# Performance work log

Hardware: AMD Instinct MI355X
Metric: run time of the kernel (lower is better)

Reference implementation:

```python
import jax, jax.numpy as jnp
import numpy as np

D_MODEL = 1024
NUM_HEADS = 16
D_STATE = D_MODEL // NUM_HEADS
BS, SEQ = 8, 1024
NEG_BIG = 1e10


def setup_inputs() -> dict:
    key = jax.random.key(0)
    ks = jax.random.split(key, 3)
    std = 0.02
    x = jax.random.normal(ks[0], (BS, SEQ, D_MODEL), dtype=jnp.float32)
    qkv_w = jax.random.normal(ks[1], (D_MODEL, 3 * D_MODEL), dtype=jnp.float32) * std
    qkv_b = jnp.zeros((3 * D_MODEL,), dtype=jnp.float32)
    out_w = jax.random.normal(ks[2], (D_MODEL, D_MODEL), dtype=jnp.float32) * std
    out_b = jnp.zeros((D_MODEL,), dtype=jnp.float32)
    return {"x": x, "qkv_w": qkv_w, "qkv_b": qkv_b, "out_w": out_w, "out_b": out_b}


def reference(x, qkv_w, qkv_b, out_w, out_b):
    bs, n, d = x.shape
    qkv = jnp.matmul(x, qkv_w) + qkv_b  # [bs, n, 3*d_model]
    q, k, v = jnp.split(qkv, 3, axis=-1)

    def split_heads(t):  # [bs, n, d] -> [bs, h, n, d_state]
        return t.reshape(bs, n, NUM_HEADS, D_STATE).transpose(0, 2, 1, 3)

    q, k, v = split_heads(q), split_heads(k), split_heads(v)
    scale = 1.0 / np.sqrt(D_STATE).astype(np.float32)
    scores = jnp.einsum('bhqd,bhkd->bhqk', q, k) * scale  # [bs,h,n,n]
    # causal mask: i >= j (mask(n) with ns==nd)
    m = (jnp.arange(n)[:, None] >= jnp.arange(n)[None, :]).astype(scores.dtype)
    scores = scores * m - (1.0 - m) * NEG_BIG
    attn = jax.nn.softmax(scores, axis=-1)
    out = jnp.einsum('bhqk,bhkd->bhqd', attn, v)  # [bs,h,n,d_state]
    out = out.transpose(0, 2, 1, 3).reshape(bs, n, d)
    return jnp.matmul(out, out_w) + out_b
```

## Files before the change

### kernel.cpp

```cpp
#include <hip/hip_runtime.h>
#include <hip/hip_bf16.h>
#include <stdint.h>

typedef __attribute__((ext_vector_type(8))) __bf16 bf16x8;
typedef __attribute__((ext_vector_type(4))) float f32x4;
typedef __attribute__((ext_vector_type(4))) unsigned int u32x4;
typedef __attribute__((ext_vector_type(4))) unsigned short u16x4;

#define SEQ 1024
#define DM 1024

#if __has_builtin(__builtin_amdgcn_exp2f)
#define EXP2(x) __builtin_amdgcn_exp2f(x)
#else
#define EXP2(x) exp2f(x)
#endif

typedef __attribute__((address_space(3))) void lds_t;
typedef __attribute__((address_space(1))) void glb_t;

__device__ __forceinline__ unsigned short f2bf(float f){
  __hip_bfloat16 h = __float2bfloat16(f);
  return __builtin_bit_cast(unsigned short, h);
}
__device__ __forceinline__ bf16x8 ld16(const unsigned short* p){
  u32x4 v = *(const u32x4*)p;
  return __builtin_bit_cast(bf16x8, v);
}
__device__ __forceinline__ void gload_lds16(const unsigned short* g, unsigned short* l){
  __builtin_amdgcn_global_load_lds((const glb_t*)g, (lds_t*)l, 16, 0, 0);
}

__global__ void cvt_f32_bf16(const float* __restrict__ in,
                             unsigned short* __restrict__ out, int n)
{
  int i = (blockIdx.x * blockDim.x + threadIdx.x) * 8;
  if (i >= n) return;
  float4 a = *(const float4*)(in + i);
  float4 b = *(const float4*)(in + i + 4);
  unsigned short v[8] = { f2bf(a.x), f2bf(a.y), f2bf(a.z), f2bf(a.w),
                          f2bf(b.x), f2bf(b.y), f2bf(b.z), f2bf(b.w) };
  *(u32x4*)(out + i) = *(u32x4*)v;
}

__global__ void transpose_cvt(const float* __restrict__ in,
                              unsigned short* __restrict__ out, int R, int C)
{
  __shared__ unsigned short t[32][33];
  int x  = blockIdx.x * 32 + threadIdx.x;
  int y0 = blockIdx.y * 32 + threadIdx.y;
#pragma unroll
  for (int i = 0; i < 32; i += 8)
    t[threadIdx.y + i][threadIdx.x] = f2bf(in[(size_t)(y0 + i) * C + x]);
  __syncthreads();
  int ox  = blockIdx.y * 32 + threadIdx.x;
  int oy0 = blockIdx.x * 32 + threadIdx.y;
#pragma unroll
  for (int i = 0; i < 32; i += 8)
    out[(size_t)(oy0 + i) * R + ox] = t[threadIdx.x][threadIdx.y + i];
}

template <int MODE>
__global__ __launch_bounds__(256, 3)
void gemm_bt(const unsigned short* __restrict__ A,
             const unsigned short* __restrict__ Bt,
             const float* __restrict__ bias,
             void* __restrict__ C0, unsigned short* __restrict__ vT,
             int M, int N, int K)
{
  __shared__ unsigned short Ls[3][2][128 * 32];
  const int tid = threadIdx.x;
  const int l = tid & 63;
  const int w = tid >> 6;

  const int nbn = N >> 7;
  const int nwg = gridDim.x;
  const int bid = blockIdx.x;
  const int qq  = nwg >> 3;
  const int sb  = (bid & 7) * qq + (bid >> 3);
  const int bm = sb / nbn, bn = sb % nbn;
  const int row0 = bm << 7, col0 = bn << 7;

  const int rA = w * 16 + (l >> 2);
  const int cS = ((l & 3) ^ ((l >> 3) & 3)) * 8;
  const unsigned short* ag = A  + (size_t)(row0 + rA) * K + cS;
  const unsigned short* bg = Bt + (size_t)(col0 + rA) * K + cS;

  auto STAGE = [&](int kt, int bi) {
    const unsigned short* a = ag + kt * 32;
    const unsigned short* b = bg + kt * 32;
    gload_lds16(a,                  &Ls[bi][0][w * 512]);
    gload_lds16(a + (size_t)64 * K, &Ls[bi][0][2048 + w * 512]);
    gload_lds16(b,                  &Ls[bi][1][w * 512]);
    gload_lds16(b + (size_t)64 * K, &Ls[bi][1][2048 + w * 512]);
  };

  const int wr = (w >> 1) * 64, wc = (w & 1) * 64;
  const f32x4 zz = {0.f, 0.f, 0.f, 0.f};
  f32x4 acc[4][4];
#pragma unroll
  for (int m = 0; m < 4; m++)
#pragma unroll
    for (int n = 0; n < 4; n++) acc[m][n] = zz;

  const int c16 = l & 15;
  const int csw = ((l >> 4) * 8) ^ (((l >> 1) & 3) << 3);

  const int NT = K >> 5;
  STAGE(0, 0);
  STAGE(1, 1);
  asm volatile("s_waitcnt vmcnt(4)" ::: "memory");
  __builtin_amdgcn_s_barrier();

  int cur = 0, stg = 2;
  for (int kt = 0; kt < NT; kt++) {
    if (kt + 2 < NT) STAGE(kt + 2, stg);

    const unsigned short* La = &Ls[cur][0][0];
    const unsigned short* Lb = &Ls[cur][1][0];
    bf16x8 af[4], bfr[4];
#pragma unroll
    for (int m = 0; m < 4; m++)
      af[m] = ld16(La + (wr + m * 16 + c16) * 32 + csw);
#pragma unroll
    for (int n = 0; n < 4; n++)
      bfr[n] = ld16(Lb + (wc + n * 16 + c16) * 32 + csw);
#pragma unroll
    for (int m = 0; m < 4; m++)
#pragma unroll
      for (int n = 0; n < 4; n++)
        acc[m][n] = __builtin_amdgcn_mfma_f32_16x16x32_bf16(af[m], bfr[n], acc[m][n], 0, 0, 0);

    if (kt + 1 < NT) {
      if (kt + 2 < NT) asm volatile("s_waitcnt vmcnt(4)" ::: "memory");
      else             asm volatile("s_waitcnt vmcnt(0)" ::: "memory");
      __builtin_amdgcn_s_barrier();
    }
    cur = (cur == 2) ? 0 : cur + 1;
    stg = (stg == 2) ? 0 : stg + 1;
  }

#pragma unroll
  for (int n = 0; n < 4; n++) {
    int col = col0 + wc + n * 16 + c16;
    float bv = bias[col];
#pragma unroll
    for (int m = 0; m < 4; m++) {
      int rbase = row0 + wr + m * 16 + (l >> 4) * 4;
      if constexpr (MODE == 2) {
#pragma unroll
        for (int r = 0; r < 4; r++)
          ((float*)C0)[(size_t)(rbase + r) * N + col] = acc[m][n][r] + bv;
      } else {
        if (col < 2048) {
          float sc = (col < 1024) ? 0.18033688f : 1.0f;
#pragma unroll
          for (int r = 0; r < 4; r++)
            ((unsigned short*)C0)[(size_t)(rbase + r) * 2048 + col] =
                f2bf((acc[m][n][r] + bv) * sc);
        } else {
          int bb = rbase >> 10, s0 = rbase & 1023;
          int hh = (col - 2048) >> 6, dd = (col - 2048) & 63;
          u16x4 pk;
#pragma unroll
          for (int r = 0; r < 4; r++) pk[r] = f2bf(acc[m][n][r] + bv);
          *(u16x4*)(vT + ((size_t)((bb * 16 + hh) * 64 + dd)) * 1024 + s0) = pk;
        }
      }
    }
  }
}

__global__ __launch_bounds__(256, 2)
void attn(const unsigned short* __restrict__ qk,
          const unsigned short* __restrict__ vT,
          unsigned short* __restrict__ ctx)
{
  __shared__ unsigned short Ksh[3][64 * 64];
  __shared__ unsigned short Ps[4][32 * 64];
  const int tid = threadIdx.x;
  const int l = tid & 63, w = tid >> 6;

  const int lin = blockIdx.x + (blockIdx.y << 2);
  const int xcd = lin & 7;
  const int j   = lin >> 3;
  const int bh  = xcd * 16 + (j & 15);
  const int bx  = j >> 4;
  const int b = bh >> 4, h = bh & 15;

  const unsigned short* qbase = qk + (size_t)b * SEQ * 2048;
  const unsigned short* kbase = qbase + 1024 + h * 64;
  const unsigned short* vbase = vT + (size_t)bh * 64 * 1024;
  unsigned short* Psw = Ps[w];
  const int d8 = (l >> 4) * 8;
  const int c16 = l & 15;
  const int r4 = (l >> 4) * 4;
  const int kvr = w * 8 + (l >> 3);
  const int cb  = (l & 7) * 16;

  const int qbA = 7 - bx, qbB = bx;
  const int q0A = qbA * 128 + w * 32, q0B = qbB * 128 + w * 32;
  const int ntA = (qbA + 1) * 2;
  const int kmaxA = (q0A + 31) >> 6, kmaxB = (q0B + 31) >> 6;

  bf16x8 qaA[2][2], qaB[2][2];
#pragma unroll
  for (int qc = 0; qc < 2; qc++)
#pragma unroll
    for (int kg = 0; kg < 2; kg++) {
      qaA[qc][kg] = ld16(qbase + (size_t)(q0A + qc * 16 + c16) * 2048
                               + h * 64 + kg * 32 + d8);
      qaB[qc][kg] = ld16(qbase + (size_t)(q0B + qc * 16 + c16) * 2048
                               + h * 64 + kg * 32 + d8);
    }

  const f32x4 zz = {0.f, 0.f, 0.f, 0.f};
  f32x4 oA[2][4], oB[2][4];
#pragma unroll
  for (int m = 0; m < 2; m++)
#pragma unroll
    for (int n = 0; n < 4; n++) { oA[m][n] = zz; oB[m][n] = zz; }
  float mA[2] = {-1e30f, -1e30f}, lA[2] = {0.f, 0.f};
  float mB[2] = {-1e30f, -1e30f}, lB[2] = {0.f, 0.f};

  auto STAGEK = [&](int t, int bufi) {
#pragma unroll
    for (int i = 0; i < 2; i++) {
      int row = i * 32 + kvr;
      int srcb = cb ^ ((row & 7) << 4);
      gload_lds16(kbase + (size_t)(t * 64 + row) * 2048 + (srcb >> 1),
                  &Ksh[bufi][i * 2048 + w * 512]);
    }
  };

  auto QK = [&](const unsigned short* Kc, bf16x8 (&qa)[2][2], f32x4 (&st)[4][2]) {
    bf16x8 kb[4];
    int bo0 = ((d8) * 2) ^ ((c16 & 7) << 4);
    int bo1 = (((32 + d8)) * 2) ^ ((c16 & 7) << 4);
#pragma unroll
    for (int mt = 0; mt < 4; mt++)
      kb[mt] = ld16(Kc + (mt * 16 + c16) * 64 + (bo0 >> 1));
#pragma unroll
    for (int mt = 0; mt < 4; mt++)
#pragma unroll
      for (int qc = 0; qc < 2; qc++)
        st[mt][qc] = __builtin_amdgcn_mfma_f32_16x16x32_bf16(kb[mt], qa[qc][0], zz, 0, 0, 0);
#pragma unroll
    for (int mt = 0; mt < 4; mt++)
      kb[mt] = ld16(Kc + (mt * 16 + c16) * 64 + (bo1 >> 1));
#pragma unroll
    for (int mt = 0; mt < 4; mt++)
#pragma unroll
      for (int qc = 0; qc < 2; qc++)
        st[mt][qc] = __builtin_amdgcn_mfma_f32_16x16x32_bf16(kb[mt], qa[qc][1], st[mt][qc], 0, 0, 0);
  };

  auto SMPV = [&](f32x4 (&st)[4][2], f32x4 (&o)[2][4], float (&mrun)[2],
                  float (&lrun)[2], int q0, int kvt,
                  bf16x8 (&vb0)[4], bf16x8 (&vb1)[4]) {
    if (kvt * 64 + 63 > q0) {
#pragma unroll
      for (int mt = 0; mt < 4; mt++)
#pragma unroll
        for (int qc = 0; qc < 2; qc++) {
          int qg = q0 + qc * 16 + c16;
#pragma unroll
          for (int r = 0; r < 4; r++) {
            int kvg = kvt * 64 + mt * 16 + r4 + r;
            if (kvg > qg) st[mt][qc][r] = -1e30f;
          }
        }
    }
    float plane[2];
#pragma unroll
    for (int qc = 0; qc < 2; qc++) {
      float mx = -1e30f;
#pragma unroll
      for (int mt = 0; mt < 4; mt++)
#pragma unroll
        for (int r = 0; r < 4; r++) mx = fmaxf(mx, st[mt][qc][r]);
      plane[qc] = mx;
    }
    int defer0 = __all(plane[0] - mrun[0] <= 11.5f);
    int defer1 = __all(plane[1] - mrun[1] <= 11.5f);
    float scq[2] = {1.f, 1.f};
#pragma unroll
    for (int qc = 0; qc < 2; qc++) {
      int defer = qc ? defer1 : defer0;
      if (!defer) {
        float mx = plane[qc];
        mx = fmaxf(mx, __shfl_xor(mx, 16));
        mx = fmaxf(mx, __shfl_xor(mx, 32));
        float mn = fmaxf(mrun[qc], mx);
        scq[qc] = EXP2(mrun[qc] - mn);
        mrun[qc] = mn;
      }
      float mn = mrun[qc];
      float rs = 0.f;
#pragma unroll
      for (int mt = 0; mt < 4; mt++)
#pragma unroll
        for (int r = 0; r < 4; r++) {
          float p = EXP2(st[mt][qc][r] - mn);
          st[mt][qc][r] = p;
          rs += p;
        }
      rs += __shfl_xor(rs, 16);
      rs += __shfl_xor(rs, 32);
      lrun[qc] = lrun[qc] * scq[qc] + rs;
    }
    if (!(defer0 && defer1)) {
#pragma unroll
      for (int m = 0; m < 2; m++)
#pragma unroll
        for (int r = 0; r < 4; r++) {
          float sc = __shfl(scq[m], (l & 48) | (r4 + r));
#pragma unroll
          for (int n = 0; n < 4; n++) o[m][n][r] *= sc;
        }
    }
#pragma unroll
    for (int qc = 0; qc < 2; qc++) {
      int rowl = qc * 16 + c16;
#pragma unroll
      for (int mt = 0; mt < 4; mt++) {
        int byteoff = ((mt * 16 + r4) * 2) ^ ((c16 & 7) << 4);
        u16x4 pk;
#pragma unroll
        for (int r = 0; r < 4; r++) pk[r] = f2bf(st[mt][qc][r]);
        *(u16x4*)(Psw + rowl * 64 + (byteoff >> 1)) = pk;
      }
    }
    bf16x8 pa[2];
    int bo0 = (d8 * 2) ^ ((c16 & 7) << 4);
    int bo1 = ((32 + d8) * 2) ^ ((c16 & 7) << 4);
#pragma unroll
    for (int m = 0; m < 2; m++)
      pa[m] = ld16(Psw + (m * 16 + c16) * 64 + (bo0 >> 1));
#pragma unroll
    for (int m = 0; m < 2; m++)
#pragma unroll
      for (int n = 0; n < 4; n++)
        o[m][n] = __builtin_amdgcn_mfma_f32_16x16x32_bf16(pa[m], vb0[n], o[m][n], 0, 0, 0);
#pragma unroll
    for (int m = 0; m < 2; m++)
      pa[m] = ld16(Psw + (m * 16 + c16) * 64 + (bo1 >> 1));
#pragma unroll
    for (int m = 0; m < 2; m++)
#pragma unroll
      for (int n = 0; n < 4; n++)
        o[m][n] = __builtin_amdgcn_mfma_f32_16x16x32_bf16(pa[m], vb1[n], o[m][n], 0, 0, 0);
  };

  STAGEK(0, 0);
  STAGEK(1, 1);
  asm volatile("s_waitcnt vmcnt(2)" ::: "memory");
  __builtin_amdgcn_s_barrier();

  int bufc = 0;
  for (int kvt = 0; kvt < ntA; kvt++) {
    const int bufn = bufc ? bufc - 1 : 2;
    const bool more = (kvt + 2 < ntA);
    if (more) STAGEK(kvt + 2, bufn);
    const unsigned short* Kc = Ksh[bufc];

    if (kvt <= kmaxA) {
      f32x4 st[4][2];
      QK(Kc, qaA, st);
      bf16x8 vb0[4], vb1[4];
#pragma unroll
      for (int n = 0; n < 4; n++) {
        vb0[n] = ld16(vbase + (size_t)(n * 16 + c16) * 1024 + kvt * 64 + d8);
        vb1[n] = ld16(vbase + (size_t)(n * 16 + c16) * 1024 + kvt * 64 + 32 + d8);
      }
      SMPV(st, oA, mA, lA, q0A, kvt, vb0, vb1);
      if (kvt <= kmaxB) {
        QK(Kc, qaB, st);
        SMPV(st, oB, mB, lB, q0B, kvt, vb0, vb1);
      }
    }

    if (more) asm volatile("s_waitcnt vmcnt(2)" ::: "memory");
    else      asm volatile("s_waitcnt vmcnt(0)" ::: "memory");
    __builtin_amdgcn_s_barrier();
    bufc = (bufc == 2) ? 0 : bufc + 1;
  }

  auto WRITE = [&](f32x4 (&o)[2][4], float (&lrun)[2], int q0) {
    float invq[2];
#pragma unroll
    for (int qc = 0; qc < 2; qc++) invq[qc] = 1.f / lrun[qc];
#pragma unroll
    for (int m = 0; m < 2; m++)
#pragma unroll
      for (int r = 0; r < 4; r++) {
        float inv = __shfl(invq[m], (l & 48) | (r4 + r));
        int qg = q0 + m * 16 + r4 + r;
#pragma unroll
        for (int n = 0; n < 4; n++) {
          int d = n * 16 + c16;
          ctx[(size_t)(b * SEQ + qg) * DM + h * 64 + d] = f2bf(o[m][n][r] * inv);
        }
      }
  };
  WRITE(oA, lA, q0A);
  WRITE(oB, lB, q0B);
}

extern "C" void kernel_launch(void* const* d_in, const int* in_sizes, int n_in,
                              void* d_out, int out_size, void* d_ws, size_t ws_size,
                              hipStream_t stream)
{
  const float* x     = (const float*)d_in[0];
  const float* qkv_w = (const float*)d_in[1];
  const float* qkv_b = (const float*)d_in[2];
  const float* out_w = (const float*)d_in[3];
  const float* out_b = (const float*)d_in[4];

  unsigned short* ws   = (unsigned short*)d_ws;
  unsigned short* xb   = ws;
  unsigned short* wqT  = xb  + (size_t)8192 * 1024;
  unsigned short* woT  = wqT + 3072 * 1024;
  unsigned short* qkb  = woT + 1024 * 1024;
  unsigned short* vTb  = qkb + (size_t)8192 * 2048;
  unsigned short* ctxb = vTb + (size_t)128 * 64 * 1024;

  hipLaunchKernelGGL(cvt_f32_bf16, dim3(8192 * 1024 / 8 / 256), dim3(256), 0, stream,
                     x, xb, 8192 * 1024);
  hipLaunchKernelGGL(transpose_cvt, dim3(3072 / 32, 1024 / 32), dim3(32, 8), 0, stream,
                     qkv_w, wqT, 1024, 3072);
  hipLaunchKernelGGL(transpose_cvt, dim3(1024 / 32, 1024 / 32), dim3(32, 8), 0, stream,
                     out_w, woT, 1024, 1024);
  hipLaunchKernelGGL(gemm_bt<1>, dim3(64 * 24), dim3(256), 0, stream,
                     xb, wqT, qkv_b, (void*)qkb, vTb, 8192, 3072, 1024);
  hipLaunchKernelGGL(attn, dim3(4, 128), dim3(256), 0, stream,
                     qkb, vTb, ctxb);
  hipLaunchKernelGGL(gemm_bt<2>, dim3(64 * 8), dim3(256), 0, stream,
                     ctxb, woT, out_b, d_out, nullptr, 8192, 1024, 1024);
}
```

Baseline: 151.1 us.

## Deepen GEMM LDS pipeline to five stages and process two k-tiles per barrier

The bf16 GEMM's shared-memory ring grows from three to five buffers, with three tiles prefetched up front. Each loop iteration now issues two new tile loads and consumes two k-tiles, so it needs half as many s_barrier and waitcnt sync points. The goal is to hide global-load latency better and cut synchronization overhead in the MFMA loop. In exchange, LDS use per block rises, so launch bounds drop to two blocks per CU, and holding fragments for two tiles raises register pressure.

```diff
diff --git a/kernel.cpp b/kernel.cpp
--- a/kernel.cpp
+++ b/kernel.cpp
@@ -61,14 +61,14 @@
 }
 
 template <int MODE>
-__global__ __launch_bounds__(256, 3)
+__global__ __launch_bounds__(256, 2)
 void gemm_bt(const unsigned short* __restrict__ A,
              const unsigned short* __restrict__ Bt,
              const float* __restrict__ bias,
              void* __restrict__ C0, unsigned short* __restrict__ vT,
              int M, int N, int K)
 {
-  __shared__ unsigned short Ls[3][2][128 * 32];
+  __shared__ unsigned short Ls[5][2][128 * 32];
   const int tid = threadIdx.x;
   const int l = tid & 63;
   const int w = tid >> 6;
@@ -107,37 +107,57 @@
   const int csw = ((l >> 4) * 8) ^ (((l >> 1) & 3) << 3);
 
   const int NT = K >> 5;
+  const int NJ = NT >> 1;
   STAGE(0, 0);
   STAGE(1, 1);
+  STAGE(2, 2);
   asm volatile("s_waitcnt vmcnt(4)" ::: "memory");
   __builtin_amdgcn_s_barrier();
 
-  int cur = 0, stg = 2;
-  for (int kt = 0; kt < NT; kt++) {
-    if (kt + 2 < NT) STAGE(kt + 2, stg);
-
-    const unsigned short* La = &Ls[cur][0][0];
-    const unsigned short* Lb = &Ls[cur][1][0];
-    bf16x8 af[4], bfr[4];
+  int b0 = 0;
+  for (int j = 0; j < NJ; j++) {
+    const int t0 = j << 1;
+    const int b1 = (b0 == 4) ? 0 : b0 + 1;
+    const int s0 = (b0 >= 2) ? b0 - 2 : b0 + 3;
+    const int s1 = (b0 >= 1) ? b0 - 1 : 4;
+    const bool more2 = (t0 + 4) < NT;
+    if (t0 + 3 < NT) STAGE(t0 + 3, s0);
+    if (more2)       STAGE(t0 + 4, s1);
+
+    const unsigned short* LaA = &Ls[b0][0][0];
+    const unsigned short* LbA = &Ls[b0][1][0];
+    const unsigned short* LaB = &Ls[b1][0][0];
+    const unsigned short* LbB = &Ls[b1][1][0];
+    bf16x8 af0[4], bf0[4], af1[4], bf1[4];
 #pragma unroll
     for (int m = 0; m < 4; m++)
-      af[m] = ld16(La + (wr + m * 16 + c16) * 32 + csw);
+      af0[m] = ld16(LaA + (wr + m * 16 + c16) * 32 + csw);
 #pragma unroll
     for (int n = 0; n < 4; n++)
-      bfr[n] = ld16(Lb + (wc + n * 16 + c16) * 32 + csw);
+      bf0[n] = ld16(LbA + (wc + n * 16 + c16) * 32 + csw);
 #pragma unroll
     for (int m = 0; m < 4; m++)
+      af1[m] = ld16(LaB + (wr + m * 16 + c16) * 32 + csw);
+#pragma unroll
+    for (int n = 0; n < 4; n++)
+      bf1[n] = ld16(LbB + (wc + n * 16 + c16) * 32 + csw);
+#pragma unroll
+    for (int m = 0; m < 4; m++)
 #pragma unroll
       for (int n = 0; n < 4; n++)
-        acc[m][n] = __builtin_amdgcn_mfma_f32_16x16x32_bf16(af[m], bfr[n], acc[m][n], 0, 0, 0);
-
-    if (kt + 1 < NT) {
-      if (kt + 2 < NT) asm volatile("s_waitcnt vmcnt(4)" ::: "memory");
-      else             asm volatile("s_waitcnt vmcnt(0)" ::: "memory");
+        acc[m][n] = __builtin_amdgcn_mfma_f32_16x16x32_bf16(af0[m], bf0[n], acc[m][n], 0, 0, 0);
+#pragma unroll
+    for (int m = 0; m < 4; m++)
+#pragma unroll
+      for (int n = 0; n < 4; n++)
+        acc[m][n] = __builtin_amdgcn_mfma_f32_16x16x32_bf16(af1[m], bf1[n], acc[m][n], 0, 0, 0);
+
+    if (j + 1 < NJ) {
+      if (more2) asm volatile("s_waitcnt vmcnt(4)" ::: "memory");
+      else       asm volatile("s_waitcnt vmcnt(0)" ::: "memory");
       __builtin_amdgcn_s_barrier();
     }
-    cur = (cur == 2) ? 0 : cur + 1;
-    stg = (stg == 2) ? 0 : stg + 1;
+    b0 = (b0 >= 3) ? b0 - 3 : b0 + 2;
   }
 
 #pragma unroll
@@ -159,12 +179,12 @@
             ((unsigned short*)C0)[(size_t)(rbase + r) * 2048 + col] =
                 f2bf((acc[m][n][r] + bv) * sc);
         } else {
-          int bb = rbase >> 10, s0 = rbase & 1023;
+          int bb = rbase >> 10, s0v = rbase & 1023;
           int hh = (col - 2048) >> 6, dd = (col - 2048) & 63;
           u16x4 pk;
 #pragma unroll
           for (int r = 0; r < 4; r++) pk[r] = f2bf(acc[m][n][r] + bv);
-          *(u16x4*)(vT + ((size_t)((bb * 16 + hh) * 64 + dd)) * 1024 + s0) = pk;
+          *(u16x4*)(vT + ((size_t)((bb * 16 + hh) * 64 + dd)) * 1024 + s0v) = pk;
         }
       }
     }
```

Measured after the change: 152.4 us. Within noise of the previous version (+0.8%).

## Use 256x256 tile, 512-thread, 4-stage pipelined QKV GEMM kernel

Applied to the files above, without the earlier changes.

Replaces the templated 128x128 GEMM for the QKV projection with a dedicated kernel using 256x256 output tiles, 8 waves of 512 threads, and a 4-deep LDS prefetch pipeline. Each wave computes a 128x64 sub-tile, so more MFMA work is done per LDS load and global traffic per output is lower. The output projection keeps the old 128x128 kernel, now specialized without the mode template. The cost is fewer workgroups (384), which can leave CUs underused, plus 64KB of LDS and higher register pressure per block.

```diff
diff --git a/kernel.cpp b/kernel.cpp
--- a/kernel.cpp
+++ b/kernel.cpp
@@ -60,13 +60,123 @@
     out[(size_t)(oy0 + i) * R + ox] = t[threadIdx.x][threadIdx.y + i];
 }
 
-template <int MODE>
+__global__ __launch_bounds__(512, 2)
+void gemm_qkv(const unsigned short* __restrict__ A,
+              const unsigned short* __restrict__ Bt,
+              const float* __restrict__ bias,
+              unsigned short* __restrict__ qko, unsigned short* __restrict__ vT,
+              int M, int N, int K)
+{
+  __shared__ unsigned short As[4][8192];
+  __shared__ unsigned short Bs[4][8192];
+  const int tid = threadIdx.x;
+  const int l = tid & 63;
+  const int w = tid >> 6;
+  const int wm = w >> 2, wn = w & 3;
+
+  const int nbn = N >> 8;
+  const int nwg = gridDim.x;
+  const int bid = blockIdx.x;
+  const int qq  = nwg >> 3;
+  const int sb  = (bid & 7) * qq + (bid >> 3);
+  const int bm = sb / nbn, bn = sb % nbn;
+  const int row0 = bm << 8, col0 = bn << 8;
+
+  const int rs = tid >> 2;
+  const int cS = ((tid & 3) ^ ((tid >> 3) & 3)) * 8;
+  const unsigned short* ag = A  + (size_t)(row0 + rs) * K + cS;
+  const unsigned short* bg = Bt + (size_t)(col0 + rs) * K + cS;
+
+  auto STAGE = [&](int kt, int bi) {
+    const unsigned short* a = ag + kt * 32;
+    const unsigned short* b = bg + kt * 32;
+    gload_lds16(a,                   &As[bi][w * 512]);
+    gload_lds16(a + (size_t)128 * K, &As[bi][4096 + w * 512]);
+    gload_lds16(b,                   &Bs[bi][w * 512]);
+    gload_lds16(b + (size_t)128 * K, &Bs[bi][4096 + w * 512]);
+  };
+
+  const f32x4 zz = {0.f, 0.f, 0.f, 0.f};
+  f32x4 acc[8][4];
+#pragma unroll
+  for (int m = 0; m < 8; m++)
+#pragma unroll
+    for (int n = 0; n < 4; n++) acc[m][n] = zz;
+
+  const int c16 = l & 15;
+  const int csw = ((l >> 4) * 8) ^ (((l >> 1) & 3) << 3);
+  const int NT = K >> 5;
+
+  STAGE(0, 0);
+  STAGE(1, 1);
+  STAGE(2, 2);
+  asm volatile("s_waitcnt vmcnt(8)" ::: "memory");
+  __builtin_amdgcn_s_barrier();
+
+  for (int t = 0; t < NT; t++) {
+    const int bi = t & 3;
+    if (t + 3 < NT) STAGE(t + 3, (t + 3) & 3);
+
+    bf16x8 bfr[4], af[4];
+#pragma unroll
+    for (int n = 0; n < 4; n++)
+      bfr[n] = ld16(&Bs[bi][(wn * 64 + n * 16 + c16) * 32 + csw]);
+#pragma unroll
+    for (int m = 0; m < 4; m++)
+      af[m] = ld16(&As[bi][(wm * 128 + m * 16 + c16) * 32 + csw]);
+#pragma unroll
+    for (int m = 0; m < 4; m++)
+#pragma unroll
+      for (int n = 0; n < 4; n++)
+        acc[m][n] = __builtin_amdgcn_mfma_f32_16x16x32_bf16(af[m], bfr[n], acc[m][n], 0, 0, 0);
+
+    bf16x8 af2[4];
+#pragma unroll
+    for (int m = 0; m < 4; m++)
+      af2[m] = ld16(&As[bi][(wm * 128 + (m + 4) * 16 + c16) * 32 + csw]);
+#pragma unroll
+    for (int m = 0; m < 4; m++)
+#pragma unroll
+      for (int n = 0; n < 4; n++)
+        acc[m + 4][n] = __builtin_amdgcn_mfma_f32_16x16x32_bf16(af2[m], bfr[n], acc[m + 4][n], 0, 0, 0);
+
+    if (t + 1 < NT) {
+      if      (t + 3 < NT) asm volatile("s_waitcnt vmcnt(8)" ::: "memory");
+      else if (t + 2 < NT) asm volatile("s_waitcnt vmcnt(4)" ::: "memory");
+      else                 asm volatile("s_waitcnt vmcnt(0)" ::: "memory");
+      __builtin_amdgcn_s_barrier();
+    }
+  }
+
+#pragma unroll
+  for (int n = 0; n < 4; n++) {
+    int col = col0 + wn * 64 + n * 16 + c16;
+    float bv = bias[col];
+#pragma unroll
+    for (int m = 0; m < 8; m++) {
+      int rbase = row0 + wm * 128 + m * 16 + (l >> 4) * 4;
+      if (col < 2048) {
+        float sc = (col < 1024) ? 0.18033688f : 1.0f;
+#pragma unroll
+        for (int r = 0; r < 4; r++)
+          qko[(size_t)(rbase + r) * 2048 + col] = f2bf((acc[m][n][r] + bv) * sc);
+      } else {
+        int bb = rbase >> 10, s0v = rbase & 1023;
+        int hh = (col - 2048) >> 6, dd = (col - 2048) & 63;
+        u16x4 pk;
+#pragma unroll
+        for (int r = 0; r < 4; r++) pk[r] = f2bf(acc[m][n][r] + bv);
+        *(u16x4*)(vT + ((size_t)((bb * 16 + hh) * 64 + dd)) * 1024 + s0v) = pk;
+      }
+    }
+  }
+}
+
 __global__ __launch_bounds__(256, 3)
-void gemm_bt(const unsigned short* __restrict__ A,
-             const unsigned short* __restrict__ Bt,
-             const float* __restrict__ bias,
-             void* __restrict__ C0, unsigned short* __restrict__ vT,
-             int M, int N, int K)
+void gemm_out(const unsigned short* __restrict__ A,
+              const unsigned short* __restrict__ Bt,
+              const float* __restrict__ bias,
+              float* __restrict__ C, int M, int N, int K)
 {
   __shared__ unsigned short Ls[3][2][128 * 32];
   const int tid = threadIdx.x;
@@ -147,26 +257,9 @@
 #pragma unroll
     for (int m = 0; m < 4; m++) {
       int rbase = row0 + wr + m * 16 + (l >> 4) * 4;
-      if constexpr (MODE == 2) {
-#pragma unroll
-        for (int r = 0; r < 4; r++)
-          ((float*)C0)[(size_t)(rbase + r) * N + col] = acc[m][n][r] + bv;
-      } else {
-        if (col < 2048) {
-          float sc = (col < 1024) ? 0.18033688f : 1.0f;
-#pragma unroll
-          for (int r = 0; r < 4; r++)
-            ((unsigned short*)C0)[(size_t)(rbase + r) * 2048 + col] =
-                f2bf((acc[m][n][r] + bv) * sc);
-        } else {
-          int bb = rbase >> 10, s0 = rbase & 1023;
-          int hh = (col - 2048) >> 6, dd = (col - 2048) & 63;
-          u16x4 pk;
-#pragma unroll
-          for (int r = 0; r < 4; r++) pk[r] = f2bf(acc[m][n][r] + bv);
-          *(u16x4*)(vT + ((size_t)((bb * 16 + hh) * 64 + dd)) * 1024 + s0) = pk;
-        }
-      }
+#pragma unroll
+      for (int r = 0; r < 4; r++)
+        C[(size_t)(rbase + r) * N + col] = acc[m][n][r] + bv;
     }
   }
 }
@@ -431,10 +524,10 @@
                      qkv_w, wqT, 1024, 3072);
   hipLaunchKernelGGL(transpose_cvt, dim3(1024 / 32, 1024 / 32), dim3(32, 8), 0, stream,
                      out_w, woT, 1024, 1024);
-  hipLaunchKernelGGL(gemm_bt<1>, dim3(64 * 24), dim3(256), 0, stream,
-                     xb, wqT, qkv_b, (void*)qkb, vTb, 8192, 3072, 1024);
+  hipLaunchKernelGGL(gemm_qkv, dim3(32 * 12), dim3(512), 0, stream,
+                     xb, wqT, qkv_b, qkb, vTb, 8192, 3072, 1024);
   hipLaunchKernelGGL(attn, dim3(4, 128), dim3(256), 0, stream,
                      qkb, vTb, ctxb);
-  hipLaunchKernelGGL(gemm_bt<2>, dim3(64 * 8), dim3(256), 0, stream,
-                     ctxb, woT, out_b, d_out, nullptr, 8192, 1024, 1024);
-}
+  hipLaunchKernelGGL(gemm_out, dim3(64 * 8), dim3(256), 0, stream,
+                     ctxb, woT, out_b, (float*)d_out, 8192, 1024, 1024);
+}
```

After: 174.7 us. +15.6%, slower.
